# Kernel optimization log

Measured on AMD Instinct MI355X. Metric: run time of the kernel, lower is better.

Reference implementation:

```python
import jax, jax.numpy as jnp
import numpy as np

B, SQ, SK, D = 32, 2048, 2048, 64


def setup_inputs() -> dict:
    key = jax.random.key(0)
    kq, kk, km = jax.random.split(key, 3)
    q = jax.random.normal(kq, (B, SQ, D), dtype=jnp.float32)
    k = jax.random.normal(kk, (B, SK, D), dtype=jnp.float32)
    mask = jax.random.randint(km, (B, SQ, SK), 0, 2, dtype=jnp.int32)
    return {"q": q, "k": k, "mask": mask}


def reference(q, k, mask):
    # scores = q @ k^T / sqrt(D)  -> [B, SQ, SK]
    scale = 1.0 / np.sqrt(q.shape[-1]).astype(np.float32)
    scores = jnp.einsum('bqd,bkd->bqk', q, k) * scale
    scores = jnp.where(mask == 0, -jnp.inf, scores)
    return jax.nn.softmax(scores, axis=-1)
```

## Files before the change

kernel.cpp:

```cpp
#include <hip/hip_runtime.h>
#include <math.h>

constexpr int BB  = 32;
constexpr int SQL = 2048;
constexpr int SKL = 2048;
constexpr int DD  = 64;

using f32x4 = __attribute__((ext_vector_type(4))) float;
using bfrag = __attribute__((ext_vector_type(8))) short;
typedef unsigned long long u64;

static __device__ __forceinline__ unsigned short f2bf(float x) {
    unsigned u = __float_as_uint(x);
    u = u + 0x7FFFu + ((u >> 16) & 1u);
    return (unsigned short)(u >> 16);
}
static __device__ __forceinline__ float bf2f(unsigned short h) {
    return __uint_as_float((unsigned)h << 16);
}

static __device__ __forceinline__ void gld16(const void* g, void* l) {
    __builtin_amdgcn_global_load_lds(
        (const __attribute__((address_space(1))) void*)(size_t)g,
        (__attribute__((address_space(3))) void*)(unsigned)(size_t)l,
        16, 0, 0);
}

__global__ __launch_bounds__(256) void compress_mask(
    const int* __restrict__ m, unsigned char* __restrict__ bm)
{
    const int t = threadIdx.x;
    const size_t g0 = (size_t)blockIdx.x * 1024 + t;
    const int4* mp = (const int4*)m;
    int4 a0 = mp[(g0)       * 2], a1 = mp[(g0)       * 2 + 1];
    int4 b0 = mp[(g0 + 256) * 2], b1 = mp[(g0 + 256) * 2 + 1];
    int4 c0 = mp[(g0 + 512) * 2], c1 = mp[(g0 + 512) * 2 + 1];
    int4 d0 = mp[(g0 + 768) * 2], d1 = mp[(g0 + 768) * 2 + 1];
#define PACK8(v0, v1)                                                         \
    (unsigned char)((v0.x != 0 ? 1u : 0u)  | (v0.y != 0 ? 2u : 0u)   |        \
                    (v0.z != 0 ? 4u : 0u)  | (v0.w != 0 ? 8u : 0u)   |        \
                    (v1.x != 0 ? 16u : 0u) | (v1.y != 0 ? 32u : 0u)  |        \
                    (v1.z != 0 ? 64u : 0u) | (v1.w != 0 ? 128u : 0u))
    bm[g0]       = PACK8(a0, a1);
    bm[g0 + 256] = PACK8(b0, b1);
    bm[g0 + 512] = PACK8(c0, c1);
    bm[g0 + 768] = PACK8(d0, d1);
#undef PACK8
}

__global__ __launch_bounds__(256) void split_k1(
    const float* __restrict__ k, unsigned char* __restrict__ kswz)
{
    const int i0 = blockIdx.x * blockDim.x + threadIdx.x;
    const int g  = i0 & 7;
    const int c  = (i0 >> 3) & 2047;
    const int b  = i0 >> 14;
    const float* kp = k + ((size_t)(b * 2048 + c)) * DD + g * 8;
    bfrag h;
    #pragma unroll
    for (int j = 0; j < 8; ++j)
        h[j] = (short)f2bf(kp[j]);
    unsigned char* rec = kswz + ((size_t)(b * 2048 + c)) * 128;
    *(bfrag*)(rec + 16 * (g ^ (c & 7))) = h;
}

#define MF(A, B, C) __builtin_amdgcn_mfma_f32_16x16x32_bf16((A), (B), (C), 0, 0, 0)
#define NIB4(M) ((unsigned)((M).x ? 1u:0u) | ((M).y ? 2u:0u) |                 \
                 ((M).z ? 4u:0u) | ((M).w ? 8u:0u))

template<bool PRE>
__global__ __launch_bounds__(1024, 4) void sdpa_v19(
    const float* __restrict__ q, const float* __restrict__ k,
    const int* __restrict__ mask, const unsigned char* __restrict__ bm,
    const unsigned char* __restrict__ kswz, float* __restrict__ out)
{
    __shared__ char  kring[16][4][2048];
    __shared__ float s_red[16][2][16];

    const int t   = threadIdx.x;
    const int l   = t & 63;
    const int w   = t >> 6;
    const int lr  = l & 15;
    const int lg  = l >> 4;
    const int bid = blockIdx.x;
    const int swz = (bid & 7) * 256 + (bid >> 3);
    const int b   = swz >> 6;
    const int r0  = (swz & 63) * 32;
    const int c0  = w * 128;
    const size_t row0 = (size_t)b * SQL + (size_t)(r0 + lr);
    const size_t row1 = row0 + 16;

    u64 ba0 = 0, ba1 = 0, bb0 = 0, bb1 = 0;
    if constexpr (PRE) {
        const ulonglong2 va = *(const ulonglong2*)(bm + row0 * (SKL / 8) + w * 16);
        const ulonglong2 vb = *(const ulonglong2*)(bm + row1 * (SKL / 8) + w * 16);
        ba0 = va.x; ba1 = va.y; bb0 = vb.x; bb1 = vb.y;
    }

    constexpr float QS = 0.18033688011112042f;
    bfrag qh0a, ql0a, qh1a, ql1a;
    bfrag qh0b, ql0b, qh1b, ql1b;
#define LOADQ(ROW, H0, L0, H1, L1)                                             \
    do {                                                                       \
        const float* _qp = q + (ROW) * DD + lg * 8;                            \
        const f32x4 _x0 = *(const f32x4*)_qp;                                  \
        const f32x4 _x1 = *(const f32x4*)(_qp + 4);                            \
        const f32x4 _y0 = *(const f32x4*)(_qp + 32);                           \
        const f32x4 _y1 = *(const f32x4*)(_qp + 36);                           \
        _Pragma("unroll")                                                      \
        for (int _j = 0; _j < 4; ++_j) {                                       \
            float _a = _x0[_j] * QS, _c = _x1[_j] * QS;                        \
            float _d = _y0[_j] * QS, _e = _y1[_j] * QS;                        \
            unsigned short _h;                                                 \
            _h = f2bf(_a); H0[_j]   = (short)_h; L0[_j]   = (short)f2bf(_a - bf2f(_h)); \
            _h = f2bf(_c); H0[_j+4] = (short)_h; L0[_j+4] = (short)f2bf(_c - bf2f(_h)); \
            _h = f2bf(_d); H1[_j]   = (short)_h; L1[_j]   = (short)f2bf(_d - bf2f(_h)); \
            _h = f2bf(_e); H1[_j+4] = (short)_h; L1[_j+4] = (short)f2bf(_e - bf2f(_h)); \
        }                                                                      \
    } while (0)
    LOADQ(row0, qh0a, ql0a, qh1a, ql1a);
    LOADQ(row1, qh0b, ql0b, qh1b, ql1b);
#undef LOADQ
    __builtin_amdgcn_sched_barrier(0);

    const char*  ksrc = PRE ? (const char*)(kswz + ((size_t)b * SKL + c0) * 128) : nullptr;
    const float* kraw = PRE ? nullptr : k + (size_t)b * SKL * DD;
    const int*   mr0  = PRE ? nullptr : mask + row0 * SKL + c0 + lg * 4;
    const int*   mr1  = PRE ? nullptr : mask + row1 * SKL + c0 + lg * 4;
    char* kseg = &kring[w][0][0];

#define STAGE(T)                                                               \
    do {                                                                       \
        if constexpr (PRE) {                                                   \
            char* _kd = kseg + (((T) & 3) << 11);                              \
            const char* _ks = ksrc + (size_t)(T) * 2048;                       \
            gld16(_ks + l * 16,        _kd + l * 16);                          \
            gld16(_ks + 1024 + l * 16, _kd + 1024 + l * 16);                   \
        }                                                                      \
    } while (0)

    STAGE(0);
    STAGE(1);
    STAGE(2);

    unsigned sc[32];
    float psum0 = 0.f, psum1 = 0.f;

#define ITER(T, VMC, MW0, MW1)                                                 \
    do {                                                                       \
        bfrag _kh0, _kh1;                                                      \
        int4 _mva, _mvb;                                                       \
        if constexpr (PRE) {                                                   \
            asm volatile("s_waitcnt vmcnt(" #VMC ")" ::: "memory");            \
            const char* _c = kseg + (((T) & 3) << 11) + lr * 128;              \
            _kh0 = *(const bfrag*)(_c + 16 * (lg ^ (lr & 7)));                 \
            _kh1 = *(const bfrag*)(_c + 16 * ((4 | lg) ^ (lr & 7)));           \
            asm volatile("s_waitcnt lgkmcnt(0)" ::: "memory");                 \
            __builtin_amdgcn_sched_barrier(0);                                 \
            if constexpr ((T) + 3 < 8) STAGE((T) + 3);                         \
        } else {                                                               \
            const float* _kc = kraw + (size_t)(c0 + (T) * 16 + lr) * DD;       \
            const f32x4 _v0 = *(const f32x4*)(_kc + lg * 8);                   \
            const f32x4 _v1 = *(const f32x4*)(_kc + lg * 8 + 4);               \
            const f32x4 _v2 = *(const f32x4*)(_kc + 32 + lg * 8);              \
            const f32x4 _v3 = *(const f32x4*)(_kc + 36 + lg * 8);              \
            _Pragma("unroll")                                                  \
            for (int _j = 0; _j < 4; ++_j) {                                   \
                _kh0[_j]     = (short)f2bf(_v0[_j]);                           \
                _kh0[_j + 4] = (short)f2bf(_v1[_j]);                           \
                _kh1[_j]     = (short)f2bf(_v2[_j]);                           \
                _kh1[_j + 4] = (short)f2bf(_v3[_j]);                           \
            }                                                                  \
            _mva = *(const int4*)(mr0 + (T) * 16);                             \
            _mvb = *(const int4*)(mr1 + (T) * 16);                             \
        }                                                                      \
                              \
        f32x4 _h = {0.f, 0.f, 0.f, 0.f};                                       \
        f32x4 _m = {0.f, 0.f, 0.f, 0.f};                                       \
        _h = MF(_kh0, qh0a, _h);  _m = MF(_kh0, ql0a, _m);                     \
        _h = MF(_kh1, qh1a, _h);  _m = MF(_kh1, ql1a, _m);                     \
        const f32x4 _s0 = _h + _m;                                             \
                                                                  \
        f32x4 _h2 = {0.f, 0.f, 0.f, 0.f};                                      \
        f32x4 _m2 = {0.f, 0.f, 0.f, 0.f};                                      \
        _h2 = MF(_kh0, qh0b, _h2);  _m2 = MF(_kh0, ql0b, _m2);                 \
        _h2 = MF(_kh1, qh1b, _h2);  _m2 = MF(_kh1, ql1b, _m2);                 \
        const f32x4 _s1 = _h2 + _m2;                                           \
        unsigned _n0, _n1;                                                     \
        if constexpr (PRE) {                                                   \
            _n0 = (unsigned)((MW0) >> (((T) & 3) * 16 + lg * 4)) & 0xFu;       \
            _n1 = (unsigned)((MW1) >> (((T) & 3) * 16 + lg * 4)) & 0xFu;       \
        } else {                                                               \
            _n0 = NIB4(_mva);                                                  \
            _n1 = NIB4(_mvb);                                                  \
        }                                                                      \
        const float _e0 = (_n0 & 1u) ? exp2f(_s0[0]) : 0.f;                    \
        const float _e1 = (_n0 & 2u) ? exp2f(_s0[1]) : 0.f;                    \
        const float _e2 = (_n0 & 4u) ? exp2f(_s0[2]) : 0.f;                    \
        const float _e3 = (_n0 & 8u) ? exp2f(_s0[3]) : 0.f;                    \
        const float _f0 = (_n1 & 1u) ? exp2f(_s1[0]) : 0.f;                    \
        const float _f1 = (_n1 & 2u) ? exp2f(_s1[1]) : 0.f;                    \
        const float _f2 = (_n1 & 4u) ? exp2f(_s1[2]) : 0.f;                    \
        const float _f3 = (_n1 & 8u) ? exp2f(_s1[3]) : 0.f;                    \
        psum0 += (_e0 + _e1) + (_e2 + _e3);                                    \
        psum1 += (_f0 + _f1) + (_f2 + _f3);                                    \
        asm volatile("v_cvt_pk_bf16_f32 %0, %1, %2"                            \
                     : "=v"(sc[4 * (T)])     : "v"(_e0), "v"(_e1));            \
        asm volatile("v_cvt_pk_bf16_f32 %0, %1, %2"                            \
                     : "=v"(sc[4 * (T) + 1]) : "v"(_e2), "v"(_e3));            \
        asm volatile("v_cvt_pk_bf16_f32 %0, %1, %2"                            \
                     : "=v"(sc[4 * (T) + 2]) : "v"(_f0), "v"(_f1));            \
        asm volatile("v_cvt_pk_bf16_f32 %0, %1, %2"                            \
                     : "=v"(sc[4 * (T) + 3]) : "v"(_f2), "v"(_f3));            \
    } while (0)

    ITER(0, 4, ba0, bb0); ITER(1, 4, ba0, bb0);
    ITER(2, 4, ba0, bb0); ITER(3, 4, ba0, bb0);
    ITER(4, 4, ba1, bb1); ITER(5, 4, ba1, bb1);
    ITER(6, 2, ba1, bb1); ITER(7, 0, ba1, bb1);
#undef ITER
#undef STAGE

    psum0 += __shfl_xor(psum0, 16, 64);
    psum0 += __shfl_xor(psum0, 32, 64);
    psum1 += __shfl_xor(psum1, 16, 64);
    psum1 += __shfl_xor(psum1, 32, 64);

    if (l < 16) {
        s_red[w][0][lr] = psum0;
        s_red[w][1][lr] = psum1;
    }
    __syncthreads();

    float tot0 = 0.f, tot1 = 0.f;
    #pragma unroll
    for (int ww = 0; ww < 16; ++ww) {
        tot0 += s_red[ww][0][lr];
        tot1 += s_red[ww][1][lr];
    }
    const float rinv0 = 1.0f / tot0;
    const float rinv1 = 1.0f / tot1;

    float* op0 = out + row0 * SKL + c0 + lg * 4;
    float* op1 = out + row1 * SKL + c0 + lg * 4;
    #pragma unroll
    for (int T = 0; T < 8; ++T) {
        const unsigned pa = sc[4 * T], pb = sc[4 * T + 1];
        const unsigned pc = sc[4 * T + 2], pd = sc[4 * T + 3];
        f32x4 o0, o1;
        o0[0] = bf2f((unsigned short)(pa & 0xffffu)) * rinv0;
        o0[1] = bf2f((unsigned short)(pa >> 16))     * rinv0;
        o0[2] = bf2f((unsigned short)(pb & 0xffffu)) * rinv0;
        o0[3] = bf2f((unsigned short)(pb >> 16))     * rinv0;
        o1[0] = bf2f((unsigned short)(pc & 0xffffu)) * rinv1;
        o1[1] = bf2f((unsigned short)(pc >> 16))     * rinv1;
        o1[2] = bf2f((unsigned short)(pd & 0xffffu)) * rinv1;
        o1[3] = bf2f((unsigned short)(pd >> 16))     * rinv1;
        *reinterpret_cast<f32x4*>(op0 + T * 16) = o0;
        *reinterpret_cast<f32x4*>(op1 + T * 16) = o1;
    }
}

extern "C" void kernel_launch(void* const* d_in, const int* in_sizes, int n_in,
                              void* d_out, int out_size, void* d_ws, size_t ws_size,
                              hipStream_t stream) {
    const float* q    = (const float*)d_in[0];
    const float* k    = (const float*)d_in[1];
    const int*   mask = (const int*)d_in[2];
    float*       out  = (float*)d_out;

    const size_t BM_B = (size_t)BB * SQL * SKL / 8;
    const size_t KS_B = (size_t)BB * SKL * 128;

    dim3 grid(2048);

    if (ws_size >= BM_B + KS_B) {
        unsigned char* bmp = (unsigned char*)d_ws;
        unsigned char* ksp = (unsigned char*)d_ws + BM_B;
        compress_mask<<<16384, 256, 0, stream>>>(mask, bmp);
        split_k1<<<2048, 256, 0, stream>>>(k, ksp);
        sdpa_v19<true><<<grid, 1024, 0, stream>>>(q, k, mask, bmp, ksp, out);
    } else {
        sdpa_v19<false><<<grid, 1024, 0, stream>>>(q, k, mask, nullptr, nullptr, out);
    }
}
```

Measured before the change: 333.2 us.

## Recompute scores in a second pass instead of caching bf16 exps; halve block size

Blocks drop from 1024 to 512 threads, so each wave covers 256 key columns (16 tiles) instead of 128. Instead of keeping packed bf16 exponentials in registers between the sum pass and the write pass, the kernel recomputes the QK MFMA and exp2 in a second pass after the row-sum reduction, re-staging K through LDS. This frees the sc register array and avoids bf16 rounding of the probabilities, at the cost of doubling the matmul, exp work and K staging traffic. The vmcnt wait counts in the second pass mix pending output stores with the K loads.

```diff
diff --git a/kernel.cpp b/kernel.cpp
--- a/kernel.cpp
+++ b/kernel.cpp
@@ -69,13 +69,13 @@
                  ((M).z ? 4u:0u) | ((M).w ? 8u:0u))
 
 template<bool PRE>
-__global__ __launch_bounds__(1024, 4) void sdpa_v19(
+__global__ __launch_bounds__(512, 4) void sdpa_v21(
     const float* __restrict__ q, const float* __restrict__ k,
     const int* __restrict__ mask, const unsigned char* __restrict__ bm,
     const unsigned char* __restrict__ kswz, float* __restrict__ out)
 {
-    __shared__ char  kring[16][4][2048];
-    __shared__ float s_red[16][2][16];
+    __shared__ char  kring[8][4][2048];
+    __shared__ float s_red[8][2][16];
 
     const int t   = threadIdx.x;
     const int l   = t & 63;
@@ -86,15 +86,19 @@
     const int swz = (bid & 7) * 256 + (bid >> 3);
     const int b   = swz >> 6;
     const int r0  = (swz & 63) * 32;
-    const int c0  = w * 128;
+    const int c0  = w * 256;
     const size_t row0 = (size_t)b * SQL + (size_t)(r0 + lr);
     const size_t row1 = row0 + 16;
 
-    u64 ba0 = 0, ba1 = 0, bb0 = 0, bb1 = 0;
+    u64 ba0 = 0, ba1 = 0, ba2 = 0, ba3 = 0;
+    u64 bb0 = 0, bb1 = 0, bb2 = 0, bb3 = 0;
     if constexpr (PRE) {
-        const ulonglong2 va = *(const ulonglong2*)(bm + row0 * (SKL / 8) + w * 16);
-        const ulonglong2 vb = *(const ulonglong2*)(bm + row1 * (SKL / 8) + w * 16);
-        ba0 = va.x; ba1 = va.y; bb0 = vb.x; bb1 = vb.y;
+        const ulonglong2* wa = (const ulonglong2*)(bm + row0 * (SKL / 8) + w * 32);
+        const ulonglong2* wb = (const ulonglong2*)(bm + row1 * (SKL / 8) + w * 32);
+        const ulonglong2 va0 = wa[0], va1 = wa[1];
+        const ulonglong2 vb0 = wb[0], vb1 = wb[1];
+        ba0 = va0.x; ba1 = va0.y; ba2 = va1.x; ba3 = va1.y;
+        bb0 = vb0.x; bb1 = vb0.y; bb2 = vb1.x; bb3 = vb1.y;
     }
 
     constexpr float QS = 0.18033688011112042f;
@@ -128,6 +132,8 @@
     const int*   mr0  = PRE ? nullptr : mask + row0 * SKL + c0 + lg * 4;
     const int*   mr1  = PRE ? nullptr : mask + row1 * SKL + c0 + lg * 4;
     char* kseg = &kring[w][0][0];
+    float* op0 = out + row0 * SKL + c0 + lg * 4;
+    float* op1 = out + row1 * SKL + c0 + lg * 4;
 
 #define STAGE(T)                                                               \
     do {                                                                       \
@@ -139,25 +145,16 @@
         }                                                                      \
     } while (0)
 
-    STAGE(0);
-    STAGE(1);
-    STAGE(2);
-
-    unsigned sc[32];
-    float psum0 = 0.f, psum1 = 0.f;
-
-#define ITER(T, VMC, MW0, MW1)                                                 \
-    do {                                                                       \
+#define CORE(T, MW0, MW1)                                                      \
         bfrag _kh0, _kh1;                                                      \
         int4 _mva, _mvb;                                                       \
         if constexpr (PRE) {                                                   \
-            asm volatile("s_waitcnt vmcnt(" #VMC ")" ::: "memory");            \
             const char* _c = kseg + (((T) & 3) << 11) + lr * 128;              \
             _kh0 = *(const bfrag*)(_c + 16 * (lg ^ (lr & 7)));                 \
             _kh1 = *(const bfrag*)(_c + 16 * ((4 | lg) ^ (lr & 7)));           \
             asm volatile("s_waitcnt lgkmcnt(0)" ::: "memory");                 \
             __builtin_amdgcn_sched_barrier(0);                                 \
-            if constexpr ((T) + 3 < 8) STAGE((T) + 3);                         \
+            if constexpr ((T) + 3 < 16) STAGE((T) + 3);                        \
         } else {                                                               \
             const float* _kc = kraw + (size_t)(c0 + (T) * 16 + lr) * DD;       \
             const f32x4 _v0 = *(const f32x4*)(_kc + lg * 8);                   \
@@ -174,15 +171,11 @@
             _mva = *(const int4*)(mr0 + (T) * 16);                             \
             _mvb = *(const int4*)(mr1 + (T) * 16);                             \
         }                                                                      \
-                              \
-        f32x4 _h = {0.f, 0.f, 0.f, 0.f};                                       \
-        f32x4 _m = {0.f, 0.f, 0.f, 0.f};                                       \
+        f32x4 _h = {0.f,0.f,0.f,0.f}, _m = {0.f,0.f,0.f,0.f};                  \
         _h = MF(_kh0, qh0a, _h);  _m = MF(_kh0, ql0a, _m);                     \
         _h = MF(_kh1, qh1a, _h);  _m = MF(_kh1, ql1a, _m);                     \
         const f32x4 _s0 = _h + _m;                                             \
-                                                                  \
-        f32x4 _h2 = {0.f, 0.f, 0.f, 0.f};                                      \
-        f32x4 _m2 = {0.f, 0.f, 0.f, 0.f};                                      \
+        f32x4 _h2 = {0.f,0.f,0.f,0.f}, _m2 = {0.f,0.f,0.f,0.f};                \
         _h2 = MF(_kh0, qh0b, _h2);  _m2 = MF(_kh0, ql0b, _m2);                 \
         _h2 = MF(_kh1, qh1b, _h2);  _m2 = MF(_kh1, ql1b, _m2);                 \
         const f32x4 _s1 = _h2 + _m2;                                           \
@@ -191,74 +184,92 @@
             _n0 = (unsigned)((MW0) >> (((T) & 3) * 16 + lg * 4)) & 0xFu;       \
             _n1 = (unsigned)((MW1) >> (((T) & 3) * 16 + lg * 4)) & 0xFu;       \
         } else {                                                               \
-            _n0 = NIB4(_mva);                                                  \
-            _n1 = NIB4(_mvb);                                                  \
-        }                                                                      \
-        const float _e0 = (_n0 & 1u) ? exp2f(_s0[0]) : 0.f;                    \
-        const float _e1 = (_n0 & 2u) ? exp2f(_s0[1]) : 0.f;                    \
-        const float _e2 = (_n0 & 4u) ? exp2f(_s0[2]) : 0.f;                    \
-        const float _e3 = (_n0 & 8u) ? exp2f(_s0[3]) : 0.f;                    \
-        const float _f0 = (_n1 & 1u) ? exp2f(_s1[0]) : 0.f;                    \
-        const float _f1 = (_n1 & 2u) ? exp2f(_s1[1]) : 0.f;                    \
-        const float _f2 = (_n1 & 4u) ? exp2f(_s1[2]) : 0.f;                    \
-        const float _f3 = (_n1 & 8u) ? exp2f(_s1[3]) : 0.f;                    \
-        psum0 += (_e0 + _e1) + (_e2 + _e3);                                    \
-        psum1 += (_f0 + _f1) + (_f2 + _f3);                                    \
-        asm volatile("v_cvt_pk_bf16_f32 %0, %1, %2"                            \
-                     : "=v"(sc[4 * (T)])     : "v"(_e0), "v"(_e1));            \
-        asm volatile("v_cvt_pk_bf16_f32 %0, %1, %2"                            \
-                     : "=v"(sc[4 * (T) + 1]) : "v"(_e2), "v"(_e3));            \
-        asm volatile("v_cvt_pk_bf16_f32 %0, %1, %2"                            \
-                     : "=v"(sc[4 * (T) + 2]) : "v"(_f0), "v"(_f1));            \
-        asm volatile("v_cvt_pk_bf16_f32 %0, %1, %2"                            \
-                     : "=v"(sc[4 * (T) + 3]) : "v"(_f2), "v"(_f3));            \
-    } while (0)
-
-    ITER(0, 4, ba0, bb0); ITER(1, 4, ba0, bb0);
-    ITER(2, 4, ba0, bb0); ITER(3, 4, ba0, bb0);
-    ITER(4, 4, ba1, bb1); ITER(5, 4, ba1, bb1);
-    ITER(6, 2, ba1, bb1); ITER(7, 0, ba1, bb1);
-#undef ITER
-#undef STAGE
+            _n0 = NIB4(_mva); _n1 = NIB4(_mvb);                                \
+        }
+
+#define ITERA(T, VMC, MW0, MW1)                                                \
+    do {                                                                       \
+        if constexpr (PRE)                                                     \
+            asm volatile("s_waitcnt vmcnt(" #VMC ")" ::: "memory");            \
+        CORE(T, MW0, MW1)                                                      \
+        psum0 += ((_n0 & 1u) ? exp2f(_s0[0]) : 0.f)                            \
+               + ((_n0 & 2u) ? exp2f(_s0[1]) : 0.f)                            \
+               + ((_n0 & 4u) ? exp2f(_s0[2]) : 0.f)                            \
+               + ((_n0 & 8u) ? exp2f(_s0[3]) : 0.f);                           \
+        psum1 += ((_n1 & 1u) ? exp2f(_s1[0]) : 0.f)                            \
+               + ((_n1 & 2u) ? exp2f(_s1[1]) : 0.f)                            \
+               + ((_n1 & 4u) ? exp2f(_s1[2]) : 0.f)                            \
+               + ((_n1 & 8u) ? exp2f(_s1[3]) : 0.f);                           \
+    } while (0)
+
+#define ITERB(T, VMC, MW0, MW1)                                                \
+    do {                                                                       \
+        if constexpr (PRE)                                                     \
+            asm volatile("s_waitcnt vmcnt(" #VMC ")" ::: "memory");            \
+        CORE(T, MW0, MW1)                                                      \
+        f32x4 _o0, _o1;                                                        \
+        _o0[0] = (_n0 & 1u) ? exp2f(_s0[0]) * rinv0 : 0.f;                     \
+        _o0[1] = (_n0 & 2u) ? exp2f(_s0[1]) * rinv0 : 0.f;                     \
+        _o0[2] = (_n0 & 4u) ? exp2f(_s0[2]) * rinv0 : 0.f;                     \
+        _o0[3] = (_n0 & 8u) ? exp2f(_s0[3]) * rinv0 : 0.f;                     \
+        _o1[0] = (_n1 & 1u) ? exp2f(_s1[0]) * rinv1 : 0.f;                     \
+        _o1[1] = (_n1 & 2u) ? exp2f(_s1[1]) * rinv1 : 0.f;                     \
+        _o1[2] = (_n1 & 4u) ? exp2f(_s1[2]) * rinv1 : 0.f;                     \
+        _o1[3] = (_n1 & 8u) ? exp2f(_s1[3]) * rinv1 : 0.f;                     \
+        *(f32x4*)(op0 + (T) * 16) = _o0;                                       \
+        *(f32x4*)(op1 + (T) * 16) = _o1;                                       \
+    } while (0)
+
+    STAGE(0);
+    STAGE(1);
+    STAGE(2);
+    float psum0 = 0.f, psum1 = 0.f;
+
+    ITERA(0,  4, ba0, bb0); ITERA(1,  4, ba0, bb0);
+    ITERA(2,  4, ba0, bb0); ITERA(3,  4, ba0, bb0);
+    ITERA(4,  4, ba1, bb1); ITERA(5,  4, ba1, bb1);
+    ITERA(6,  4, ba1, bb1); ITERA(7,  4, ba1, bb1);
+    ITERA(8,  4, ba2, bb2); ITERA(9,  4, ba2, bb2);
+    ITERA(10, 4, ba2, bb2); ITERA(11, 4, ba2, bb2);
+    ITERA(12, 4, ba3, bb3); ITERA(13, 4, ba3, bb3);
+    ITERA(14, 2, ba3, bb3); ITERA(15, 0, ba3, bb3);
 
     psum0 += __shfl_xor(psum0, 16, 64);
     psum0 += __shfl_xor(psum0, 32, 64);
     psum1 += __shfl_xor(psum1, 16, 64);
     psum1 += __shfl_xor(psum1, 32, 64);
-
     if (l < 16) {
         s_red[w][0][lr] = psum0;
         s_red[w][1][lr] = psum1;
     }
     __syncthreads();
-
     float tot0 = 0.f, tot1 = 0.f;
     #pragma unroll
-    for (int ww = 0; ww < 16; ++ww) {
+    for (int ww = 0; ww < 8; ++ww) {
         tot0 += s_red[ww][0][lr];
         tot1 += s_red[ww][1][lr];
     }
     const float rinv0 = 1.0f / tot0;
     const float rinv1 = 1.0f / tot1;
-
-    float* op0 = out + row0 * SKL + c0 + lg * 4;
-    float* op1 = out + row1 * SKL + c0 + lg * 4;
-    #pragma unroll
-    for (int T = 0; T < 8; ++T) {
-        const unsigned pa = sc[4 * T], pb = sc[4 * T + 1];
-        const unsigned pc = sc[4 * T + 2], pd = sc[4 * T + 3];
-        f32x4 o0, o1;
-        o0[0] = bf2f((unsigned short)(pa & 0xffffu)) * rinv0;
-        o0[1] = bf2f((unsigned short)(pa >> 16))     * rinv0;
-        o0[2] = bf2f((unsigned short)(pb & 0xffffu)) * rinv0;
-        o0[3] = bf2f((unsigned short)(pb >> 16))     * rinv0;
-        o1[0] = bf2f((unsigned short)(pc & 0xffffu)) * rinv1;
-        o1[1] = bf2f((unsigned short)(pc >> 16))     * rinv1;
-        o1[2] = bf2f((unsigned short)(pd & 0xffffu)) * rinv1;
-        o1[3] = bf2f((unsigned short)(pd >> 16))     * rinv1;
-        *reinterpret_cast<f32x4*>(op0 + T * 16) = o0;
-        *reinterpret_cast<f32x4*>(op1 + T * 16) = o1;
-    }
+    __syncthreads();
+
+    STAGE(0);
+    STAGE(1);
+    STAGE(2);
+
+    ITERB(0,  4,  ba0, bb0); ITERB(1,  6,  ba0, bb0);
+    ITERB(2,  8,  ba0, bb0); ITERB(3,  10, ba0, bb0);
+    ITERB(4,  10, ba1, bb1); ITERB(5,  10, ba1, bb1);
+    ITERB(6,  10, ba1, bb1); ITERB(7,  10, ba1, bb1);
+    ITERB(8,  10, ba2, bb2); ITERB(9,  10, ba2, bb2);
+    ITERB(10, 10, ba2, bb2); ITERB(11, 10, ba2, bb2);
+    ITERB(12, 10, ba3, bb3); ITERB(13, 10, ba3, bb3);
+    ITERB(14, 8,  ba3, bb3); ITERB(15, 6,  ba3, bb3);
+
+#undef ITERB
+#undef ITERA
+#undef CORE
+#undef STAGE
 }
 
 extern "C" void kernel_launch(void* const* d_in, const int* in_sizes, int n_in,
@@ -279,8 +290,8 @@
         unsigned char* ksp = (unsigned char*)d_ws + BM_B;
         compress_mask<<<16384, 256, 0, stream>>>(mask, bmp);
         split_k1<<<2048, 256, 0, stream>>>(k, ksp);
-        sdpa_v19<true><<<grid, 1024, 0, stream>>>(q, k, mask, bmp, ksp, out);
+        sdpa_v21<true><<<grid, 512, 0, stream>>>(q, k, mask, bmp, ksp, out);
     } else {
-        sdpa_v19<false><<<grid, 1024, 0, stream>>>(q, k, mask, nullptr, nullptr, out);
-    }
-}
+        sdpa_v21<false><<<grid, 512, 0, stream>>>(q, k, mask, nullptr, nullptr, out);
+    }
+}
```

After: 354.6 us. 1.06x slower.
